# Optimization experiments

Hardware: AMD Instinct MI355X
Metric: run time of the kernel (lower is better)

## Reference

```python
import jax, jax.numpy as jnp
import numpy as np

GROUP_SIZE = 256
QMAX = 7.0   # int4 symmetric: clamp to [-8, 7], scale from max_abs/7
QMIN = -8.0
EPS = 1e-9


def _dequantized_weight(weight):
    """Symmetric int4 group quantization (group_size=256 along input dim),
    then dequantize. Matches group_quantize_tensor_symmetric + qc4w matmul math.
    weight: [out, in] float32."""
    O, I = weight.shape
    wg = weight.reshape(O, I // GROUP_SIZE, GROUP_SIZE)
    scale = jnp.maximum(jnp.max(jnp.abs(wg), axis=-1, keepdims=True) / QMAX, EPS)
    w_int = jnp.clip(jnp.round(wg / scale), QMIN, QMAX)
    return (w_int * scale).reshape(O, I)


def setup_inputs() -> dict:
    key = jax.random.key(0)
    k1, k2 = jax.random.split(key)
    x = jax.random.normal(k1, (1, 16, 4096), dtype=jnp.float32)
    weight = jax.random.normal(k2, (14336, 4096), dtype=jnp.float32) * 0.02
    return {"x": x, "weight": weight}


def reference(x, weight):
    # x: [1, S, I]; weight: [O, I]
    w_dq = _dequantized_weight(weight)           # [O, I]
    xs = x[0]                                    # squeeze batch (asserted == 1)
    out = jnp.einsum('si,oi->so', xs, w_dq)     # [S, O]
    return out[None, ...]                        # [1, S, O]
```

## Files before the change

### kernel.cpp

```cpp
#include <hip/hip_runtime.h>


constexpr int O_DIM  = 14336;
constexpr int I_DIM  = 4096;
constexpr int S_DIM  = 16;
constexpr int GS     = 256;
constexpr int NG     = I_DIM / GS;
constexpr int RPW    = 4;
constexpr int NWAVE  = 14;
constexpr int RPB    = RPW * NWAVE;
constexpr int PH_I   = 1024;
constexpr int NPH    = I_DIM / PH_I;
constexpr int GPP    = PH_I / GS;

__global__ __launch_bounds__(896)
void qlin_kernel(const float* __restrict__ x,
                 const float* __restrict__ w,
                 float* __restrict__ out)
{
    __shared__ float xs[S_DIM][PH_I];

    const int tid  = threadIdx.x;
    const int lane = tid & 63;
    const int wv   = tid >> 6;
    const int row0 = blockIdx.x * RPB + wv * RPW;

    const float* wp = w + (size_t)row0 * I_DIM + lane * 4;

    float acc[RPW][S_DIM];
#pragma unroll
    for (int r = 0; r < RPW; ++r)
#pragma unroll
        for (int s = 0; s < S_DIM; ++s) acc[r][s] = 0.0f;

    float4 wcur[RPW], wnext[RPW];
#pragma unroll
    for (int r = 0; r < RPW; ++r)
        wcur[r] = *reinterpret_cast<const float4*>(wp + (size_t)r * I_DIM);

    for (int p = 0; p < NPH; ++p) {
        for (int j = tid; j < S_DIM * (PH_I / 4); j += 896) {
            const int s  = j >> 8;
            const int i4 = (j & 255) * 4;
            float4 v = *reinterpret_cast<const float4*>(
                &x[(size_t)s * I_DIM + p * PH_I + i4]);
            *reinterpret_cast<float4*>(&xs[s][i4]) = v;
        }
        __syncthreads();

        for (int g = 0; g < GPP; ++g) {
            const int G = p * GPP + g;

            if (G + 1 < NG) {
#pragma unroll
                for (int r = 0; r < RPW; ++r)
                    wnext[r] = *reinterpret_cast<const float4*>(
                        wp + (size_t)r * I_DIM + (G + 1) * GS);
            }

#pragma unroll
            for (int r = 0; r < RPW; ++r) {
                float4 v = wcur[r];
                float m = fmaxf(fmaxf(fabsf(v.x), fabsf(v.y)),
                                fmaxf(fabsf(v.z), fabsf(v.w)));
#pragma unroll
                for (int off = 1; off < 64; off <<= 1)
                    m = fmaxf(m, __shfl_xor(m, off, 64));
                float scale = fmaxf(m * (1.0f / 7.0f), 1e-9f);
                float invs  = 1.0f / scale;
                wcur[r].x = rintf(v.x * invs) * scale;
                wcur[r].y = rintf(v.y * invs) * scale;
                wcur[r].z = rintf(v.z * invs) * scale;
                wcur[r].w = rintf(v.w * invs) * scale;
            }

            const int xb = g * GS + lane * 4;
#pragma unroll
            for (int s = 0; s < S_DIM; ++s) {
                float4 xv = *reinterpret_cast<const float4*>(&xs[s][xb]);
#pragma unroll
                for (int r = 0; r < RPW; ++r) {
                    acc[r][s] = fmaf(wcur[r].x, xv.x, acc[r][s]);
                    acc[r][s] = fmaf(wcur[r].y, xv.y, acc[r][s]);
                    acc[r][s] = fmaf(wcur[r].z, xv.z, acc[r][s]);
                    acc[r][s] = fmaf(wcur[r].w, xv.w, acc[r][s]);
                }
            }

#pragma unroll
            for (int r = 0; r < RPW; ++r) wcur[r] = wnext[r];
        }
        __syncthreads();
    }

    float a[64];
#pragma unroll
    for (int r = 0; r < RPW; ++r)
#pragma unroll
        for (int s = 0; s < S_DIM; ++s) a[(r << 4) | s] = acc[r][s];

#pragma unroll
    for (int m = 32; m >= 1; m >>= 1) {
        const bool hi = (lane & m) != 0;
#pragma unroll
        for (int j = 0; j < m; ++j) {
            float snd  = hi ? a[j] : a[j + m];
            float rcv  = __shfl_xor(snd, m, 64);
            float kept = hi ? a[j + m] : a[j];
            a[j] = kept + rcv;
        }
    }
    {
        const int r = lane >> 4, s = lane & 15;
        out[s * O_DIM + (row0 + r)] = a[0];
    }
}

extern "C" void kernel_launch(void* const* d_in, const int* in_sizes, int n_in,
                              void* d_out, int out_size, void* d_ws, size_t ws_size,
                              hipStream_t stream) {
    const float* x = (const float*)d_in[0];
    const float* w = (const float*)d_in[1];
    float* out = (float*)d_out;
    dim3 grid(O_DIM / RPB);
    dim3 block(896);
    qlin_kernel<<<grid, block, 0, stream>>>(x, w, out);
}
```

Baseline: 339.9 us.

## Double-buffer weight groups, use DPP wave max, halve block size

Restructures the weight pipeline into two register buffers so one group's loads are in flight while the other is dequantized and used in FMAs, two groups ahead. The shuffle-based wave max reduction is replaced by DPP row operations plus a readlane. Blocks shrink from 14 to 7 waves with a launch-bounds occupancy hint of 4, which doubles the grid, and the x tile load is reordered so the first tile overlaps the initial weight loads. This adds register pressure from the extra buffer, and the smaller blocks mean each block loads the x tile separately.

```diff
diff --git a/kernel.cpp b/kernel.cpp
--- a/kernel.cpp
+++ b/kernel.cpp
@@ -7,13 +7,32 @@
 constexpr int GS     = 256;
 constexpr int NG     = I_DIM / GS;
 constexpr int RPW    = 4;
-constexpr int NWAVE  = 14;
+constexpr int NWAVE  = 7;
 constexpr int RPB    = RPW * NWAVE;
+constexpr int NTHR   = 64 * NWAVE;
 constexpr int PH_I   = 1024;
 constexpr int NPH    = I_DIM / PH_I;
 constexpr int GPP    = PH_I / GS;
 
-__global__ __launch_bounds__(896)
+__device__ __forceinline__ float wave_max_dpp(float x) {
+    int v = __float_as_int(x);
+    int t;
+    t = __builtin_amdgcn_update_dpp(0, v, 0x111, 0xf, 0xf, true);
+    v = __float_as_int(fmaxf(__int_as_float(v), __int_as_float(t)));
+    t = __builtin_amdgcn_update_dpp(0, v, 0x112, 0xf, 0xf, true);
+    v = __float_as_int(fmaxf(__int_as_float(v), __int_as_float(t)));
+    t = __builtin_amdgcn_update_dpp(0, v, 0x114, 0xf, 0xf, true);
+    v = __float_as_int(fmaxf(__int_as_float(v), __int_as_float(t)));
+    t = __builtin_amdgcn_update_dpp(0, v, 0x118, 0xf, 0xf, true);
+    v = __float_as_int(fmaxf(__int_as_float(v), __int_as_float(t)));
+    t = __builtin_amdgcn_update_dpp(0, v, 0x142, 0xf, 0xf, true);
+    v = __float_as_int(fmaxf(__int_as_float(v), __int_as_float(t)));
+    t = __builtin_amdgcn_update_dpp(0, v, 0x143, 0xf, 0xf, true);
+    v = __float_as_int(fmaxf(__int_as_float(v), __int_as_float(t)));
+    return __int_as_float(__builtin_amdgcn_readlane(v, 63));
+}
+
+__global__ __launch_bounds__(NTHR, 4)
 void qlin_kernel(const float* __restrict__ x,
                  const float* __restrict__ w,
                  float* __restrict__ out)
@@ -33,64 +52,77 @@
 #pragma unroll
         for (int s = 0; s < S_DIM; ++s) acc[r][s] = 0.0f;
 
-    float4 wcur[RPW], wnext[RPW];
+    float4 u[RPW], v[RPW];
+
+    auto loadw = [&](int G, float4* dst) {
 #pragma unroll
-    for (int r = 0; r < RPW; ++r)
-        wcur[r] = *reinterpret_cast<const float4*>(wp + (size_t)r * I_DIM);
+        for (int r = 0; r < RPW; ++r)
+            dst[r] = *reinterpret_cast<const float4*>(
+                wp + (size_t)r * I_DIM + (size_t)G * GS);
+    };
+    auto dequant = [&](float4* b) {
+#pragma unroll
+        for (int r = 0; r < RPW; ++r) {
+            float4 t = b[r];
+            float m = fmaxf(fmaxf(fabsf(t.x), fabsf(t.y)),
+                            fmaxf(fabsf(t.z), fabsf(t.w)));
+            m = wave_max_dpp(m);
+            float scale = fmaxf(m * (1.0f / 7.0f), 1e-9f);
+            float invs  = 1.0f / scale;
+            b[r].x = rintf(t.x * invs) * scale;
+            b[r].y = rintf(t.y * invs) * scale;
+            b[r].z = rintf(t.z * invs) * scale;
+            b[r].w = rintf(t.w * invs) * scale;
+        }
+    };
+    auto fmagrp = [&](const float4* b, int gloc) {
+        const int xb = gloc * GS + lane * 4;
+#pragma unroll
+        for (int s = 0; s < S_DIM; ++s) {
+            float4 xv = *reinterpret_cast<const float4*>(&xs[s][xb]);
+#pragma unroll
+            for (int r = 0; r < RPW; ++r) {
+                acc[r][s] = fmaf(b[r].x, xv.x, acc[r][s]);
+                acc[r][s] = fmaf(b[r].y, xv.y, acc[r][s]);
+                acc[r][s] = fmaf(b[r].z, xv.z, acc[r][s]);
+                acc[r][s] = fmaf(b[r].w, xv.w, acc[r][s]);
+            }
+        }
+    };
+
+    loadw(0, u);
+    loadw(1, v);
+    for (int j = tid; j < S_DIM * (PH_I / 4); j += NTHR) {
+        const int s  = j >> 8;
+        const int i4 = (j & 255) * 4;
+        *reinterpret_cast<float4*>(&xs[s][i4]) =
+            *reinterpret_cast<const float4*>(&x[(size_t)s * I_DIM + i4]);
+    }
+    dequant(u);
+    __syncthreads();
 
     for (int p = 0; p < NPH; ++p) {
-        for (int j = tid; j < S_DIM * (PH_I / 4); j += 896) {
-            const int s  = j >> 8;
-            const int i4 = (j & 255) * 4;
-            float4 v = *reinterpret_cast<const float4*>(
-                &x[(size_t)s * I_DIM + p * PH_I + i4]);
-            *reinterpret_cast<float4*>(&xs[s][i4]) = v;
+        if (p) {
+            __syncthreads();
+            for (int j = tid; j < S_DIM * (PH_I / 4); j += NTHR) {
+                const int s  = j >> 8;
+                const int i4 = (j & 255) * 4;
+                *reinterpret_cast<float4*>(&xs[s][i4]) =
+                    *reinterpret_cast<const float4*>(
+                        &x[(size_t)s * I_DIM + p * PH_I + i4]);
+            }
+            __syncthreads();
         }
-        __syncthreads();
-
-        for (int g = 0; g < GPP; ++g) {
+#pragma unroll
+        for (int g = 0; g < GPP; g += 2) {
             const int G = p * GPP + g;
-
-            if (G + 1 < NG) {
-#pragma unroll
-                for (int r = 0; r < RPW; ++r)
-                    wnext[r] = *reinterpret_cast<const float4*>(
-                        wp + (size_t)r * I_DIM + (G + 1) * GS);
-            }
-
-#pragma unroll
-            for (int r = 0; r < RPW; ++r) {
-                float4 v = wcur[r];
-                float m = fmaxf(fmaxf(fabsf(v.x), fabsf(v.y)),
-                                fmaxf(fabsf(v.z), fabsf(v.w)));
-#pragma unroll
-                for (int off = 1; off < 64; off <<= 1)
-                    m = fmaxf(m, __shfl_xor(m, off, 64));
-                float scale = fmaxf(m * (1.0f / 7.0f), 1e-9f);
-                float invs  = 1.0f / scale;
-                wcur[r].x = rintf(v.x * invs) * scale;
-                wcur[r].y = rintf(v.y * invs) * scale;
-                wcur[r].z = rintf(v.z * invs) * scale;
-                wcur[r].w = rintf(v.w * invs) * scale;
-            }
-
-            const int xb = g * GS + lane * 4;
-#pragma unroll
-            for (int s = 0; s < S_DIM; ++s) {
-                float4 xv = *reinterpret_cast<const float4*>(&xs[s][xb]);
-#pragma unroll
-                for (int r = 0; r < RPW; ++r) {
-                    acc[r][s] = fmaf(wcur[r].x, xv.x, acc[r][s]);
-                    acc[r][s] = fmaf(wcur[r].y, xv.y, acc[r][s]);
-                    acc[r][s] = fmaf(wcur[r].z, xv.z, acc[r][s]);
-                    acc[r][s] = fmaf(wcur[r].w, xv.w, acc[r][s]);
-                }
-            }
-
-#pragma unroll
-            for (int r = 0; r < RPW; ++r) wcur[r] = wnext[r];
+            fmagrp(u, g);
+            if (G + 2 < NG) loadw(G + 2, u);
+            dequant(v);
+            fmagrp(v, g + 1);
+            if (G + 3 < NG) loadw(G + 3, v);
+            if (G + 2 < NG) dequant(u);
         }
-        __syncthreads();
     }
 
     float a[64];
@@ -123,6 +155,6 @@
     const float* w = (const float*)d_in[1];
     float* out = (float*)d_out;
     dim3 grid(O_DIM / RPB);
-    dim3 block(896);
+    dim3 block(NTHR);
     qlin_kernel<<<grid, block, 0, stream>>>(x, w, out);
 }
```

New measurement: 967.6 us. +184.7%, slower.

## Use DPP wave max reduction, halve block size, and drop the trailing barrier

Applied to the files above, without the earlier changes.

Replaces the six shuffle-based xor steps of the per-group max-abs reduction with DPP row operations (row shifts, row_bcast15/31) followed by a readlane, which avoids LDS-backed ds_bpermute traffic. Block size drops from 14 to 7 waves, so the grid doubles to 512 blocks and each block has fewer waves waiting at barriers. The barrier after each phase is moved to the start of the next phase, removing one barrier per block. Smaller blocks mean the x tile is staged into LDS by more blocks, and the readlane adds a scalar dependency.

```diff
diff --git a/kernel.cpp b/kernel.cpp
--- a/kernel.cpp
+++ b/kernel.cpp
@@ -7,13 +7,32 @@
 constexpr int GS     = 256;
 constexpr int NG     = I_DIM / GS;
 constexpr int RPW    = 4;
-constexpr int NWAVE  = 14;
+constexpr int NWAVE  = 7;
+constexpr int NTHR   = 64 * NWAVE;
 constexpr int RPB    = RPW * NWAVE;
 constexpr int PH_I   = 1024;
 constexpr int NPH    = I_DIM / PH_I;
 constexpr int GPP    = PH_I / GS;
 
-__global__ __launch_bounds__(896)
+__device__ __forceinline__ float wave_max_dpp(float x) {
+    int v = __float_as_int(x);
+    int t;
+    t = __builtin_amdgcn_update_dpp(0, v, 0x111, 0xf, 0xf, true);
+    v = __float_as_int(fmaxf(__int_as_float(v), __int_as_float(t)));
+    t = __builtin_amdgcn_update_dpp(0, v, 0x112, 0xf, 0xf, true);
+    v = __float_as_int(fmaxf(__int_as_float(v), __int_as_float(t)));
+    t = __builtin_amdgcn_update_dpp(0, v, 0x114, 0xf, 0xf, true);
+    v = __float_as_int(fmaxf(__int_as_float(v), __int_as_float(t)));
+    t = __builtin_amdgcn_update_dpp(0, v, 0x118, 0xf, 0xf, true);
+    v = __float_as_int(fmaxf(__int_as_float(v), __int_as_float(t)));
+    t = __builtin_amdgcn_update_dpp(0, v, 0x142, 0xf, 0xf, true);
+    v = __float_as_int(fmaxf(__int_as_float(v), __int_as_float(t)));
+    t = __builtin_amdgcn_update_dpp(0, v, 0x143, 0xf, 0xf, true);
+    v = __float_as_int(fmaxf(__int_as_float(v), __int_as_float(t)));
+    return __int_as_float(__builtin_amdgcn_readlane(v, 63));
+}
+
+__global__ __launch_bounds__(NTHR)
 void qlin_kernel(const float* __restrict__ x,
                  const float* __restrict__ w,
                  float* __restrict__ out)
@@ -39,12 +58,13 @@
         wcur[r] = *reinterpret_cast<const float4*>(wp + (size_t)r * I_DIM);
 
     for (int p = 0; p < NPH; ++p) {
-        for (int j = tid; j < S_DIM * (PH_I / 4); j += 896) {
+        if (p) __syncthreads();
+        for (int j = tid; j < S_DIM * (PH_I / 4); j += NTHR) {
             const int s  = j >> 8;
             const int i4 = (j & 255) * 4;
-            float4 v = *reinterpret_cast<const float4*>(
-                &x[(size_t)s * I_DIM + p * PH_I + i4]);
-            *reinterpret_cast<float4*>(&xs[s][i4]) = v;
+            *reinterpret_cast<float4*>(&xs[s][i4]) =
+                *reinterpret_cast<const float4*>(
+                    &x[(size_t)s * I_DIM + p * PH_I + i4]);
         }
         __syncthreads();
 
@@ -63,9 +83,7 @@
                 float4 v = wcur[r];
                 float m = fmaxf(fmaxf(fabsf(v.x), fabsf(v.y)),
                                 fmaxf(fabsf(v.z), fabsf(v.w)));
-#pragma unroll
-                for (int off = 1; off < 64; off <<= 1)
-                    m = fmaxf(m, __shfl_xor(m, off, 64));
+                m = wave_max_dpp(m);
                 float scale = fmaxf(m * (1.0f / 7.0f), 1e-9f);
                 float invs  = 1.0f / scale;
                 wcur[r].x = rintf(v.x * invs) * scale;
@@ -90,7 +108,6 @@
 #pragma unroll
             for (int r = 0; r < RPW; ++r) wcur[r] = wnext[r];
         }
-        __syncthreads();
     }
 
     float a[64];
@@ -123,6 +140,6 @@
     const float* w = (const float*)d_in[1];
     float* out = (float*)d_out;
     dim3 grid(O_DIM / RPB);
-    dim3 block(896);
+    dim3 block(NTHR);
     qlin_kernel<<<grid, block, 0, stream>>>(x, w, out);
 }
```

New measurement: 336.7 us. About the same (-0.9%).
